# Optimization experiments

Measured on AMD Instinct MI355X. Metric: run time of the kernel, lower is better.

The kernel has to match this reference:

```python
import jax, jax.numpy as jnp
import numpy as np


def _bitlinear(x, W, b):
    # BitNet 1.58 absmean ternary quantization with STE.
    gamma = jnp.abs(W).mean() + 1e-8
    w_tern = jnp.clip(jnp.round(W / gamma), -1.0, 1.0)
    # STE: forward uses ternary weights, gradient flows to W.
    w_ste = w_tern + (W - jax.lax.stop_gradient(W))
    return x @ w_ste.T + b


def _gelu(x):
    return jax.nn.gelu(x, approximate=False)  # torch nn.GELU default is exact erf


def setup_inputs() -> dict:
    key = jax.random.key(0)
    ks = jax.random.split(key, 16)
    B, H = 8192, 2048
    dims = [2048, 1024, 512, 256]  # encoder: 2048->1024->512->256
    inp = {
        "z": jax.random.normal(ks[0], (B, H // 2), jnp.float32),
        "attention_out": jax.random.normal(ks[1], (B, H // 2), jnp.float32),
    }
    ki = 2
    for l in range(3):
        inp[f"We{l}"] = jax.random.normal(ks[ki], (dims[l + 1], dims[l]), jnp.float32) * 0.02
        inp[f"be{l}"] = jnp.zeros((dims[l + 1],), jnp.float32)
        ki += 1
    inp["Wb"] = jax.random.normal(ks[ki], (256, 256), jnp.float32) * 0.02
    inp["bb"] = jnp.zeros((256,), jnp.float32)
    ki += 1
    for l in range(3):  # decoder: 256->512->1024->2048
        inp[f"Wd{l}"] = jax.random.normal(ks[ki], (dims[2 - l], dims[3 - l]), jnp.float32) * 0.02
        inp[f"bd{l}"] = jnp.zeros((dims[2 - l],), jnp.float32)
        ki += 1
    return inp


def reference(z, attention_out, We0, be0, We1, be1, We2, be2, Wb, bb,
              Wd0, bd0, Wd1, bd1, Wd2, bd2):
    x = jnp.concatenate([z, attention_out], axis=-1)  # (B, 2048)
    skips = []
    for W, b in [(We0, be0), (We1, be1), (We2, be2)]:
        x = _gelu(_bitlinear(x, W, b))
        skips.append(x)
    x = _gelu(_bitlinear(x, Wb, bb))
    for i, (W, b) in enumerate([(Wd0, bd0), (Wd1, bd1), (Wd2, bd2)]):
        x = _bitlinear(x, W, b)
        skip = skips[-(i + 1)]
        if x.shape[-1] == skip.shape[-1]:  # static dim check; never true for this config
            x = x + skip
        x = _gelu(x)
    return x
```

## Files before the change

kernel.cpp:

```cpp
#include <hip/hip_runtime.h>
#include <hip/hip_bf16.h>
#include <cstdint>

typedef __attribute__((ext_vector_type(8))) __bf16 bf16x8;
typedef __attribute__((ext_vector_type(4))) float f32x4;

typedef __attribute__((address_space(1))) const void g_void;
typedef __attribute__((address_space(3))) void l_void;

__device__ __forceinline__ void gload_lds16(const void* g, void* l) {
  __builtin_amdgcn_global_load_lds((g_void*)(uintptr_t)g,
                                   (l_void*)(uint32_t)(uintptr_t)l, 16, 0, 0);
}

__device__ __forceinline__ ushort f2bf(float f) {
  union { float f; uint32_t u; } v; v.f = f;
  uint32_t r = v.u + 0x7fffu + ((v.u >> 16) & 1u);
  return (ushort)(r >> 16);
}

struct WDesc {
  const float* W[7];
  int nvec[7];
  int vcum[8];
};

__global__ void absmean_concat(WDesc wd, float* __restrict__ partials,
                               const float* __restrict__ z,
                               const float* __restrict__ att,
                               ushort* __restrict__ cat) {
  const int b = blockIdx.x;
  const int t = threadIdx.x;
  if (b < 448) {
    __shared__ float red[256];
    const int layer = b >> 6, blk = b & 63;
    const float4* W = (const float4*)wd.W[layer];
    const int nv = wd.nvec[layer];
    float s = 0.f;
    for (int i = blk * 256 + t; i < nv; i += 64 * 256) {
      float4 w = W[i];
      s += fabsf(w.x) + fabsf(w.y) + fabsf(w.z) + fabsf(w.w);
    }
    red[t] = s;
    __syncthreads();
    for (int o = 128; o > 0; o >>= 1) {
      if (t < o) red[t] += red[t + o];
      __syncthreads();
    }
    if (t == 0) partials[layer * 64 + blk] = red[0];
  } else {
    const int bc = b - 448;
    const int row = bc >> 1;
    const int h = bc & 1;
    const float* src = (h ? att : z) + (size_t)row * 1024 + t * 4;
    float4 a = *(const float4*)src;
    ushort4 o;
    o.x = f2bf(a.x); o.y = f2bf(a.y); o.z = f2bf(a.z); o.w = f2bf(a.w);
    *(ushort4*)(cat + (size_t)row * 2048 + h * 1024 + t * 4) = o;
  }
}

__global__ void quant_final(WDesc wd, const float* __restrict__ partials,
                            ushort* __restrict__ qw) {
  __shared__ float igs;
  const int t = threadIdx.x;
  const int v = blockIdx.x * 256 + t;
  const int v0 = blockIdx.x * 256;
  int layer = 0;
#pragma unroll
  for (int i = 1; i < 7; ++i) layer += (v0 >= wd.vcum[i]);
  if (t < 64) {
    float x = partials[layer * 64 + t];
    for (int o = 32; o > 0; o >>= 1) x += __shfl_down(x, o, 64);
    if (t == 0) {
      float mean = x / (float)(wd.nvec[layer] * 4);
      igs = 1.0f / (mean + 1e-8f);
    }
  }
  __syncthreads();
  if (v >= wd.vcum[7]) return;
  const float g = igs;
  const int lv = v - wd.vcum[layer];
  float4 w = ((const float4*)wd.W[layer])[lv];
  ushort4 o;
  o.x = f2bf(fmaxf(-1.f, fminf(1.f, rintf(w.x * g))));
  o.y = f2bf(fmaxf(-1.f, fminf(1.f, rintf(w.y * g))));
  o.z = f2bf(fmaxf(-1.f, fminf(1.f, rintf(w.z * g))));
  o.w = f2bf(fmaxf(-1.f, fminf(1.f, rintf(w.w * g))));
  ((ushort4*)qw)[v] = o;
}

__device__ __forceinline__ float gelu_fast(float x) {
  float x2 = x * x;
  float u = x * fmaf(x2, 0.0356774081f, 0.7978845608f);
  float e = exp2f(u * 2.8853900818f);
  float r = __builtin_amdgcn_rcpf(e + 1.0f);
  return x - x * r;
}

#define SB0() __builtin_amdgcn_sched_barrier(0)
#define BAR() __builtin_amdgcn_s_barrier()
#define VMW(NN) asm volatile("s_waitcnt vmcnt(%0)" ::"n"(NN) : "memory")

template <bool OUT_F32>
__device__ __forceinline__ void store4(void* Cv, int N, int row, int col0,
                                       const f32x4& av, const float4& bv) {
  float g0 = gelu_fast(av[0] + bv.x);
  float g1 = gelu_fast(av[1] + bv.y);
  float g2 = gelu_fast(av[2] + bv.z);
  float g3 = gelu_fast(av[3] + bv.w);
  if (OUT_F32) {
    float4 o = {g0, g1, g2, g3};
    *(float4*)&(((float*)Cv)[(size_t)row * N + col0]) = o;
  } else {
    ushort4 o;
    o.x = f2bf(g0); o.y = f2bf(g1); o.z = f2bf(g2); o.w = f2bf(g3);
    *(ushort4*)&(((ushort*)Cv)[(size_t)row * N + col0]) = o;
  }
}

template <int BN, bool OUT_F32>
__global__ __launch_bounds__(512, 2)
void gemm_pipe3(const ushort* __restrict__ A, const ushort* __restrict__ Bw,
                const float* __restrict__ bias, void* __restrict__ Cv,
                int M, int N, int K) {
  constexpr int BM = 256;
  constexpr int WN = BN / 4;
  constexpr int FM = 8;
  constexpr int FN = WN / 16;
  constexpr int HM = 4;
  constexpr int HN = 1;
  constexpr int SA = 4;
  constexpr int SB = BN / 64;
  constexpr int L = SA + SB;
  constexpr int TILE_USH = (BM + BN) * 64;

  __shared__ ushort lds[3 * TILE_USH];

  const int t = threadIdx.x;
  const int lane = t & 63, wid = t >> 6;
  const int wr = wid >> 2, wc = wid & 3;
  const int l15 = lane & 15, lhi = lane >> 4;

  const int gx = gridDim.x;
  const int nwg = gx * gridDim.y;
  int lin = blockIdx.y * gx + blockIdx.x;
  lin = (lin & 7) * (nwg >> 3) + (lin >> 3);
  const int bm0 = (lin / gx) * BM, bn0 = (lin % gx) * BN;

  const int NT = K >> 6;

  const int srow = t >> 3;
  const int scol = ((t & 7) ^ ((t >> 3) & 7)) * 8;

  auto stage = [&](int tile, int buf) {
    ushort* tb = &lds[buf * TILE_USH];
    const int kt = tile * 64;
#pragma unroll
    for (int c = 0; c < SA; ++c) {
      const int lr = c * 64 + srow;
      gload_lds16(A + (size_t)(bm0 + lr) * K + kt + scol,
                  &tb[lr * 64 + (t & 7) * 8]);
    }
#pragma unroll
    for (int c = 0; c < SB; ++c) {
      const int lr = c * 64 + srow;
      gload_lds16(Bw + (size_t)(bn0 + lr) * K + kt + scol,
                  &tb[BM * 64 + lr * 64 + (t & 7) * 8]);
    }
  };

  bf16x8 a[HM][2], b[HN][2];
  f32x4 acc[FM][FN] = {};

  auto loadA = [&](const ushort* tb, int mh) {
#pragma unroll
    for (int mi = 0; mi < HM; ++mi) {
      const int row = wr * 128 + (mh * HM + mi) * 16 + l15;
#pragma unroll
      for (int kh = 0; kh < 2; ++kh)
        a[mi][kh] =
            *(const bf16x8*)&tb[row * 64 + ((kh * 4 + lhi) ^ (l15 & 7)) * 8];
    }
  };
  auto loadB = [&](const ushort* tb, int nh) {
#pragma unroll
    for (int ni = 0; ni < HN; ++ni) {
      const int row = wc * WN + (nh * HN + ni) * 16 + l15;
#pragma unroll
      for (int kh = 0; kh < 2; ++kh)
        b[ni][kh] = *(const bf16x8*)&tb[BM * 64 + row * 64 +
                                        ((kh * 4 + lhi) ^ (l15 & 7)) * 8];
    }
  };

#define MFMA_(MH, NH)                                                        \
  {                                                                          \
    _Pragma("unroll") for (int kh = 0; kh < 2; ++kh)                         \
    _Pragma("unroll") for (int mi = 0; mi < HM; ++mi)                        \
    _Pragma("unroll") for (int ni = 0; ni < HN; ++ni)                        \
      acc[(MH) * HM + mi][(NH) * HN + ni] =                                  \
          __builtin_amdgcn_mfma_f32_16x16x32_bf16(                           \
              b[ni][kh], a[mi][kh], acc[(MH) * HM + mi][(NH) * HN + ni],     \
              0, 0, 0);                                                      \
  }

  stage(0, 0);
  stage(1, 1);
  VMW(L);
  BAR();

  int buf = 0, sbuf = 2;
  for (int tt = 0; tt < NT; ++tt) {
    const bool more = (tt + 2 < NT);
    if (more) stage(tt + 2, sbuf);
    const ushort* tb = &lds[buf * TILE_USH];
    if constexpr (FN == 2) {
      loadA(tb, 0); loadB(tb, 0);
      MFMA_(0, 0);
      loadB(tb, 1);
      MFMA_(0, 1);
      loadA(tb, 1);
      MFMA_(1, 1);
      loadB(tb, 0);
      MFMA_(1, 0);
    } else {
      loadA(tb, 0); loadB(tb, 0);
      MFMA_(0, 0);
      loadA(tb, 1);
      MFMA_(1, 0);
    }
    if (more) { VMW(L); } else { VMW(0); }
    BAR();
    buf = (buf == 2) ? 0 : buf + 1;
    sbuf = (sbuf == 2) ? 0 : sbuf + 1;
  }
#undef MFMA_

#pragma unroll
  for (int m = 0; m < FM; ++m) {
    const int row = bm0 + wr * 128 + m * 16 + l15;
#pragma unroll
    for (int n = 0; n < FN; ++n) {
      const int col0 = bn0 + wc * WN + n * 16 + lhi * 4;
      const float4 bv = *(const float4*)&bias[col0];
      store4<OUT_F32>(Cv, N, row, col0, acc[m][n], bv);
    }
  }
}

template <bool OUT_F32>
__global__ __launch_bounds__(512, 2)
void gemm_8p2(const ushort* __restrict__ A, const ushort* __restrict__ Bw,
              const float* __restrict__ bias, void* __restrict__ Cv,
              int M, int N, int K) {
  constexpr int BM = 256;
  constexpr int BN = 256;
  constexpr int TILE_USH = (BM + BN) * 64;

  __shared__ ushort lds[2 * TILE_USH];

  const int t = threadIdx.x;
  const int lane = t & 63, wid = t >> 6;
  const int wr = wid >> 2, wc = wid & 3;
  const int l15 = lane & 15, lhi = lane >> 4;

  const int gx = gridDim.x;
  const int nwg = gx * gridDim.y;
  int lin = blockIdx.y * gx + blockIdx.x;
  lin = (lin & 7) * (nwg >> 3) + (lin >> 3);
  const int bm0 = (lin / gx) * BM, bn0 = (lin % gx) * BN;

  const int NT = K >> 6;

  const int srow = t >> 3;
  const int scol = ((t & 7) ^ ((t >> 3) & 7)) * 8;

  auto stageA = [&](ushort* tb, int kt, int h) {
#pragma unroll
    for (int c = 0; c < 2; ++c) {
      const int lr = h * 128 + c * 64 + srow;
      gload_lds16(A + (size_t)(bm0 + lr) * K + kt * 64 + scol,
                  &tb[lr * 64 + (t & 7) * 8]);
    }
  };
  auto stageB = [&](ushort* tb, int kt, int h) {
#pragma unroll
    for (int c = 0; c < 2; ++c) {
      const int lr = h * 128 + c * 64 + srow;
      gload_lds16(Bw + (size_t)(bn0 + lr) * K + kt * 64 + scol,
                  &tb[BM * 64 + lr * 64 + (t & 7) * 8]);
    }
  };

  bf16x8 a[2][4][2];
  bf16x8 b[2][2][2];
  f32x4 acc[8][4] = {};

  auto loadA = [&](const ushort* tb, int mh) {
#pragma unroll
    for (int mi = 0; mi < 4; ++mi) {
      const int row = wr * 128 + mh * 64 + mi * 16 + l15;
#pragma unroll
      for (int kh = 0; kh < 2; ++kh)
        a[mh][mi][kh] =
            *(const bf16x8*)&tb[row * 64 + ((kh * 4 + lhi) ^ (l15 & 7)) * 8];
    }
  };
  auto loadB = [&](const ushort* tb, int nh) {
#pragma unroll
    for (int ni = 0; ni < 2; ++ni) {
      const int row = wc * 64 + nh * 32 + ni * 16 + l15;
#pragma unroll
      for (int kh = 0; kh < 2; ++kh)
        b[nh][ni][kh] = *(const bf16x8*)&tb[BM * 64 + row * 64 +
                                            ((kh * 4 + lhi) ^ (l15 & 7)) * 8];
    }
  };

#define MFMA_(MH, NH)                                                        \
  {                                                                          \
    __builtin_amdgcn_s_setprio(1);                                           \
    _Pragma("unroll") for (int kh = 0; kh < 2; ++kh)                         \
    _Pragma("unroll") for (int mi = 0; mi < 4; ++mi)                         \
    _Pragma("unroll") for (int ni = 0; ni < 2; ++ni)                         \
      acc[(MH) * 4 + mi][(NH) * 2 + ni] =                                    \
          __builtin_amdgcn_mfma_f32_16x16x32_bf16(                           \
              b[(NH)][ni][kh], a[(MH)][mi][kh],                              \
              acc[(MH) * 4 + mi][(NH) * 2 + ni], 0, 0, 0);                   \
    __builtin_amdgcn_s_setprio(0);                                           \
  }

  {
    ushort* b0 = &lds[0];
    ushort* b1 = &lds[TILE_USH];
    stageA(b0, 0, 0); stageA(b0, 0, 1);
    stageB(b0, 0, 0); stageB(b0, 0, 1);
    stageA(b1, 1, 0); stageA(b1, 1, 1);
    VMW(4);
    BAR();
  }

  for (int J = 0; J < NT; ++J) {
    const ushort* tb = &lds[(J & 1) * TILE_USH];
    ushort* cb = &lds[(J & 1) * TILE_USH];
    ushort* sb = &lds[((J + 1) & 1) * TILE_USH];
    const bool s1 = (J + 1) < NT;
    const bool s2 = (J + 2) < NT;

    loadA(tb, 0);
    loadB(tb, 0);
    if (s1) stageB(sb, J + 1, 0);
    MFMA_(0, 0);
    loadA(tb, 1);
    loadB(tb, 1);
    if (s1) stageB(sb, J + 1, 1);
    MFMA_(1, 1);
    SB0();
    BAR();
    if (s2) { stageA(cb, J + 2, 0); stageA(cb, J + 2, 1); }
    MFMA_(0, 1);
    MFMA_(1, 0);
    if (s2) { VMW(4); } else { VMW(0); }
    BAR();
  }
#undef MFMA_

#pragma unroll
  for (int m = 0; m < 8; ++m) {
    const int row = bm0 + wr * 128 + m * 16 + l15;
#pragma unroll
    for (int n = 0; n < 4; ++n) {
      const int col0 = bn0 + wc * 64 + n * 16 + lhi * 4;
      const float4 bv = *(const float4*)&bias[col0];
      store4<OUT_F32>(Cv, N, row, col0, acc[m][n], bv);
    }
  }
}

__global__ __launch_bounds__(256, 3)
void gemm_l2l3(const ushort* __restrict__ A, const ushort* __restrict__ W2,
               const float* __restrict__ b2, const ushort* __restrict__ W3,
               const float* __restrict__ b3, ushort* __restrict__ C) {
  __shared__ ushort As[32 * 64];
  __shared__ ushort Bs[256 * 64];
  __shared__ ushort X[32 * 256];
  const int t = threadIdx.x;
  const int lane = t & 63, wid = t >> 6;
  const int wr = wid >> 1, wc = wid & 1;
  const int l15 = lane & 15, lhi = lane >> 4;
  const int bm0 = blockIdx.x * 32;
  const int arow = wr * 16 + l15;
  const int sw = (arow & 7) << 3;

  f32x4 acc[8] = {};

  for (int kt = 0; kt < 512; kt += 64) {
    {
      int r = t >> 3, c8 = t & 7;
      gload_lds16(A + (size_t)(bm0 + r) * 512 + kt + c8 * 8, &As[t * 8]);
    }
#pragma unroll
    for (int i = 0; i < 8; ++i) {
      int c = i * 256 + t;
      int r = c >> 3, c8 = c & 7;
      gload_lds16(W2 + (size_t)r * 512 + kt + c8 * 8, &Bs[c * 8]);
    }
    asm volatile("s_waitcnt vmcnt(0)" ::: "memory");
    __syncthreads();
#pragma unroll
    for (int kk = 0; kk < 64; kk += 32) {
      bf16x8 af = *(const bf16x8*)&As[arow * 64 + kk + lhi * 8];
#pragma unroll
      for (int n = 0; n < 8; ++n) {
        bf16x8 bfr =
            *(const bf16x8*)&Bs[(wc * 128 + n * 16 + l15) * 64 + kk + lhi * 8];
        acc[n] = __builtin_amdgcn_mfma_f32_16x16x32_bf16(bfr, af, acc[n], 0, 0, 0);
      }
    }
    __syncthreads();
  }

#pragma unroll
  for (int n = 0; n < 8; ++n) {
    const int col0 = wc * 128 + n * 16 + lhi * 4;
    const float4 bv = *(const float4*)&b2[col0];
    ushort4 o;
    o.x = f2bf(gelu_fast(acc[n][0] + bv.x));
    o.y = f2bf(gelu_fast(acc[n][1] + bv.y));
    o.z = f2bf(gelu_fast(acc[n][2] + bv.z));
    o.w = f2bf(gelu_fast(acc[n][3] + bv.w));
    *(ushort4*)&X[arow * 256 + (col0 ^ sw)] = o;
    acc[n][0] = 0.f; acc[n][1] = 0.f; acc[n][2] = 0.f; acc[n][3] = 0.f;
  }
  __syncthreads();

  for (int kt = 0; kt < 256; kt += 64) {
#pragma unroll
    for (int i = 0; i < 8; ++i) {
      int c = i * 256 + t;
      int r = c >> 3, c8 = c & 7;
      gload_lds16(W3 + (size_t)r * 256 + kt + c8 * 8, &Bs[c * 8]);
    }
    asm volatile("s_waitcnt vmcnt(0)" ::: "memory");
    __syncthreads();
#pragma unroll
    for (int kk = 0; kk < 64; kk += 32) {
      bf16x8 af = *(const bf16x8*)&X[arow * 256 + ((kt + kk + lhi * 8) ^ sw)];
#pragma unroll
      for (int n = 0; n < 8; ++n) {
        bf16x8 bfr =
            *(const bf16x8*)&Bs[(wc * 128 + n * 16 + l15) * 64 + kk + lhi * 8];
        acc[n] = __builtin_amdgcn_mfma_f32_16x16x32_bf16(bfr, af, acc[n], 0, 0, 0);
      }
    }
    __syncthreads();
  }

#pragma unroll
  for (int n = 0; n < 8; ++n) {
    const int col0 = wc * 128 + n * 16 + lhi * 4;
    const float4 bv = *(const float4*)&b3[col0];
    store4<false>(C, 256, bm0 + arow, col0, acc[n], bv);
  }
}

template <int BM, int BN, bool OUT_F32>
__global__ __launch_bounds__(256, 4)
void gemm_bt_bias_gelu(const ushort* __restrict__ A, const ushort* __restrict__ Bw,
                       const float* __restrict__ bias, void* __restrict__ Cv,
                       int M, int N, int K) {
  constexpr int WTM = BM / 32;
  constexpr int WTN = BN / 32;
  __shared__ ushort As[BM * 64];
  __shared__ ushort Bs[BN * 64];
  const int t = threadIdx.x;
  const int lane = t & 63, wid = t >> 6;
  const int wr = wid >> 1, wc = wid & 1;
  const int l15 = lane & 15, lhi = lane >> 4;

  const int gx = gridDim.x;
  const int nwg = gx * gridDim.y;
  int lin = blockIdx.y * gx + blockIdx.x;
  if ((nwg & 7) == 0) lin = (lin & 7) * (nwg >> 3) + (lin >> 3);
  const int bm0 = (lin / gx) * BM, bn0 = (lin % gx) * BN;

  const ushort* Abase = A + (size_t)bm0 * K;
  const ushort* Bbase = Bw + (size_t)bn0 * K;

  f32x4 acc[WTM][WTN] = {};

  for (int kt = 0; kt < K; kt += 64) {
#pragma unroll
    for (int i = 0; i < BM / 32; ++i) {
      int c = i * 256 + t;
      int r = c >> 3, c8 = c & 7;
      gload_lds16(Abase + (size_t)r * K + kt + c8 * 8, &As[c * 8]);
    }
#pragma unroll
    for (int i = 0; i < BN / 32; ++i) {
      int c = i * 256 + t;
      int r = c >> 3, c8 = c & 7;
      gload_lds16(Bbase + (size_t)r * K + kt + c8 * 8, &Bs[c * 8]);
    }
    asm volatile("s_waitcnt vmcnt(0)" ::: "memory");
    __syncthreads();
#pragma unroll
    for (int kk = 0; kk < 64; kk += 32) {
      bf16x8 af[WTM], bfr[WTN];
#pragma unroll
      for (int m = 0; m < WTM; ++m)
        af[m] = *(const bf16x8*)&As[(wr * (BM / 2) + m * 16 + l15) * 64 + kk + lhi * 8];
#pragma unroll
      for (int n = 0; n < WTN; ++n)
        bfr[n] = *(const bf16x8*)&Bs[(wc * (BN / 2) + n * 16 + l15) * 64 + kk + lhi * 8];
#pragma unroll
      for (int m = 0; m < WTM; ++m)
#pragma unroll
        for (int n = 0; n < WTN; ++n)
          acc[m][n] = __builtin_amdgcn_mfma_f32_16x16x32_bf16(bfr[n], af[m], acc[m][n], 0, 0, 0);
    }
    __syncthreads();
  }

#pragma unroll
  for (int m = 0; m < WTM; ++m) {
    const int row = bm0 + wr * (BM / 2) + m * 16 + l15;
#pragma unroll
    for (int n = 0; n < WTN; ++n) {
      const int col0 = bn0 + wc * (BN / 2) + n * 16 + lhi * 4;
      const float4 bv = *(const float4*)&bias[col0];
      store4<OUT_F32>(Cv, N, row, col0, acc[m][n], bv);
    }
  }
}

extern "C" void kernel_launch(void* const* d_in, const int* in_sizes, int n_in,
                              void* d_out, int out_size, void* d_ws, size_t ws_size,
                              hipStream_t stream) {
  const float* z   = (const float*)d_in[0];
  const float* att = (const float*)d_in[1];
  const float* Wptr[7] = {(const float*)d_in[2],  (const float*)d_in[4],
                          (const float*)d_in[6],  (const float*)d_in[8],
                          (const float*)d_in[10], (const float*)d_in[12],
                          (const float*)d_in[14]};
  const float* bptr[7] = {(const float*)d_in[3],  (const float*)d_in[5],
                          (const float*)d_in[7],  (const float*)d_in[9],
                          (const float*)d_in[11], (const float*)d_in[13],
                          (const float*)d_in[15]};
  const int Ns[7] = {1024, 512, 256, 256, 512, 1024, 2048};
  const int Ks[7] = {2048, 1024, 512, 256, 256, 512, 1024};
  const int M = 8192;

  char* ws = (char*)d_ws;
  ushort* bufA = (ushort*)ws;
  ushort* bufB = (ushort*)(ws + 33554432);
  ushort* qw   = (ushort*)(ws + 33554432 + 16777216);
  float* partials = (float*)(ws + 33554432 + 16777216 + 11141120);

  WDesc wd;
  int cum = 0;
  size_t qoff[7]; size_t qc = 0;
  for (int l = 0; l < 7; ++l) {
    wd.W[l] = Wptr[l];
    int nv = Ns[l] * Ks[l] / 4;
    wd.nvec[l] = nv;
    wd.vcum[l] = cum;
    cum += nv;
    qoff[l] = qc;
    qc += (size_t)Ns[l] * Ks[l];
  }
  wd.vcum[7] = cum;

  const int qblks = (cum + 255) / 256;
  absmean_concat<<<448 + 16384, 256, 0, stream>>>(wd, partials, z, att, bufA);
  quant_final<<<qblks, 256, 0, stream>>>(wd, partials, qw);

  ushort* inb = bufA; ushort* outb = bufB;
  gemm_pipe3<128, false><<<dim3(Ns[0] / 128, M / 256), dim3(512), 0, stream>>>(
      inb, qw + qoff[0], bptr[0], outb, M, Ns[0], Ks[0]);
  { ushort* tmp = inb; inb = outb; outb = tmp; }
  gemm_pipe3<64, false><<<dim3(Ns[1] / 64, M / 256), dim3(512), 0, stream>>>(
      inb, qw + qoff[1], bptr[1], outb, M, Ns[1], Ks[1]);
  { ushort* tmp = inb; inb = outb; outb = tmp; }
  gemm_l2l3<<<M / 32, 256, 0, stream>>>(
      inb, qw + qoff[2], bptr[2], qw + qoff[3], bptr[3], outb);
  { ushort* tmp = inb; inb = outb; outb = tmp; }
  gemm_pipe3<64, false><<<dim3(Ns[4] / 64, M / 256), dim3(512), 0, stream>>>(
      inb, qw + qoff[4], bptr[4], outb, M, Ns[4], Ks[4]);
  { ushort* tmp = inb; inb = outb; outb = tmp; }
  gemm_pipe3<128, false><<<dim3(Ns[5] / 128, M / 256), dim3(512), 0, stream>>>(
      inb, qw + qoff[5], bptr[5], outb, M, Ns[5], Ks[5]);
  { ushort* tmp = inb; inb = outb; outb = tmp; }
  gemm_8p2<true><<<dim3(Ns[6] / 256, M / 256), dim3(512), 0, stream>>>(
      inb, qw + qoff[6], bptr[6], d_out, M, Ns[6], Ks[6]);
}
```

Before: 173.9 us.

## Fuse first decoder layer into bottleneck l2/l3 kernel

The bottleneck kernel now keeps the GELU'd layer-3 output as bf16 in the LDS X tile. It then computes the 256->512 decoder layer in two 256-column halves inside the same block, instead of writing the activation to global memory and launching a separate tiled GEMM. This removes one kernel launch and a global round-trip of the 256-wide intermediate activation. In exchange, the new layer runs with the fused kernel's small 32-row tiles and unpipelined synchronous weight loads. Every block reloads the full 512x256 weight matrix, which adds L2 traffic and may lower MFMA efficiency compared with the dedicated GEMM.

```diff
diff --git a/kernel.cpp b/kernel.cpp
--- a/kernel.cpp
+++ b/kernel.cpp
@@ -379,9 +379,10 @@
 }
 
 __global__ __launch_bounds__(256, 3)
-void gemm_l2l3(const ushort* __restrict__ A, const ushort* __restrict__ W2,
-               const float* __restrict__ b2, const ushort* __restrict__ W3,
-               const float* __restrict__ b3, ushort* __restrict__ C) {
+void gemm_l2l3l4(const ushort* __restrict__ A, const ushort* __restrict__ W2,
+                 const float* __restrict__ b2, const ushort* __restrict__ Wb,
+                 const float* __restrict__ b3, const ushort* __restrict__ W4,
+                 const float* __restrict__ b4, ushort* __restrict__ C) {
   __shared__ ushort As[32 * 64];
   __shared__ ushort Bs[256 * 64];
   __shared__ ushort X[32 * 256];
@@ -440,7 +441,7 @@
     for (int i = 0; i < 8; ++i) {
       int c = i * 256 + t;
       int r = c >> 3, c8 = c & 7;
-      gload_lds16(W3 + (size_t)r * 256 + kt + c8 * 8, &Bs[c * 8]);
+      gload_lds16(Wb + (size_t)r * 256 + kt + c8 * 8, &Bs[c * 8]);
     }
     asm volatile("s_waitcnt vmcnt(0)" ::: "memory");
     __syncthreads();
@@ -461,7 +462,47 @@
   for (int n = 0; n < 8; ++n) {
     const int col0 = wc * 128 + n * 16 + lhi * 4;
     const float4 bv = *(const float4*)&b3[col0];
-    store4<false>(C, 256, bm0 + arow, col0, acc[n], bv);
+    ushort4 o;
+    o.x = f2bf(gelu_fast(acc[n][0] + bv.x));
+    o.y = f2bf(gelu_fast(acc[n][1] + bv.y));
+    o.z = f2bf(gelu_fast(acc[n][2] + bv.z));
+    o.w = f2bf(gelu_fast(acc[n][3] + bv.w));
+    *(ushort4*)&X[arow * 256 + (col0 ^ sw)] = o;
+  }
+
+#pragma unroll
+  for (int nh = 0; nh < 2; ++nh) {
+#pragma unroll
+    for (int n = 0; n < 8; ++n) {
+      acc[n][0] = 0.f; acc[n][1] = 0.f; acc[n][2] = 0.f; acc[n][3] = 0.f;
+    }
+    for (int kt = 0; kt < 256; kt += 64) {
+#pragma unroll
+      for (int i = 0; i < 8; ++i) {
+        int c = i * 256 + t;
+        int r = c >> 3, c8 = c & 7;
+        gload_lds16(W4 + (size_t)(nh * 256 + r) * 256 + kt + c8 * 8, &Bs[c * 8]);
+      }
+      asm volatile("s_waitcnt vmcnt(0)" ::: "memory");
+      __syncthreads();
+#pragma unroll
+      for (int kk = 0; kk < 64; kk += 32) {
+        bf16x8 af = *(const bf16x8*)&X[arow * 256 + ((kt + kk + lhi * 8) ^ sw)];
+#pragma unroll
+        for (int n = 0; n < 8; ++n) {
+          bf16x8 bfr =
+              *(const bf16x8*)&Bs[(wc * 128 + n * 16 + l15) * 64 + kk + lhi * 8];
+          acc[n] = __builtin_amdgcn_mfma_f32_16x16x32_bf16(bfr, af, acc[n], 0, 0, 0);
+        }
+      }
+      __syncthreads();
+    }
+#pragma unroll
+    for (int n = 0; n < 8; ++n) {
+      const int col0 = wc * 128 + n * 16 + lhi * 4;
+      const float4 bv = *(const float4*)&b4[nh * 256 + col0];
+      store4<false>(C, 512, bm0 + arow, nh * 256 + col0, acc[n], bv);
+    }
   }
 }
 
@@ -583,11 +624,9 @@
   gemm_pipe3<64, false><<<dim3(Ns[1] / 64, M / 256), dim3(512), 0, stream>>>(
       inb, qw + qoff[1], bptr[1], outb, M, Ns[1], Ks[1]);
   { ushort* tmp = inb; inb = outb; outb = tmp; }
-  gemm_l2l3<<<M / 32, 256, 0, stream>>>(
-      inb, qw + qoff[2], bptr[2], qw + qoff[3], bptr[3], outb);
-  { ushort* tmp = inb; inb = outb; outb = tmp; }
-  gemm_pipe3<64, false><<<dim3(Ns[4] / 64, M / 256), dim3(512), 0, stream>>>(
-      inb, qw + qoff[4], bptr[4], outb, M, Ns[4], Ks[4]);
+  gemm_l2l3l4<<<M / 32, 256, 0, stream>>>(
+      inb, qw + qoff[2], bptr[2], qw + qoff[3], bptr[3],
+      qw + qoff[4], bptr[4], outb);
   { ushort* tmp = inb; inb = outb; outb = tmp; }
   gemm_pipe3<128, false><<<dim3(Ns[5] / 128, M / 256), dim3(512), 0, stream>>>(
       inb, qw + qoff[5], bptr[5], outb, M, Ns[5], Ks[5]);
```

New measurement: 176.7 us. About the same (+1.6%).
